# Optimization experiments

Hardware: AMD Instinct MI355X
Metric: run time of the kernel (lower is better)

## Reference

```python
import jax, jax.numpy as jnp
import numpy as np

N_NODES = 100000
N_EDGES = 1600000
N_PAIRS = 200000
IN_C, HID_C, OUT_C = 128, 128, 64


def setup_inputs() -> dict:
    key = jax.random.key(0)
    ks = jax.random.split(key, 10)
    x = jax.random.normal(ks[0], (N_NODES, IN_C), dtype=jnp.float32)
    edge_index = jax.random.randint(ks[1], (2, N_EDGES), 0, N_NODES, dtype=jnp.int64)
    node_i = jax.random.randint(ks[2], (N_PAIRS,), 0, N_NODES, dtype=jnp.int64)
    node_j = jax.random.randint(ks[3], (N_PAIRS,), 0, N_NODES, dtype=jnp.int64)
    def glorot(k, fan_in, fan_out):
        s = jnp.sqrt(6.0 / (fan_in + fan_out))
        return jax.random.uniform(k, (fan_in, fan_out), jnp.float32, -s, s)
    W1 = glorot(ks[4], IN_C, HID_C)
    b1 = jnp.zeros((HID_C,), jnp.float32)
    W2 = glorot(ks[5], HID_C, HID_C)
    b2 = jnp.zeros((HID_C,), jnp.float32)
    W3 = glorot(ks[6], HID_C, OUT_C)
    b3 = jnp.zeros((OUT_C,), jnp.float32)
    return {"x": x, "edge_index": edge_index, "node_i": node_i, "node_j": node_j,
            "W1": W1, "b1": b1, "W2": W2, "b2": b2, "W3": W3, "b3": b3}


def _gcn_layer(h, src, dst, deg_inv, w_e, W, b):
    # h: [N, Cin] -> linear then symmetric-normalized aggregation (with self loops)
    h = h @ W  # [N, Cout]
    msg = h[src] * w_e[:, None]  # [E, Cout] gather + edge weight
    agg = jax.ops.segment_sum(msg, dst, num_segments=N_NODES)
    agg = agg + h * deg_inv[:, None]  # self-loop term: h_i / deg_i
    return agg + b


def reference(x, edge_index, node_i, node_j, W1, b1, W2, b2, W3, b3):
    src, dst = edge_index[0], edge_index[1]
    # GCN normalization with self loops: deg_i = 1 + in-degree
    ones = jnp.ones((N_EDGES,), jnp.float32)
    deg = jax.ops.segment_sum(ones, dst, num_segments=N_NODES) + 1.0
    dinv_sqrt = jax.lax.rsqrt(deg)
    deg_inv = 1.0 / deg
    w_e = dinv_sqrt[src] * dinv_sqrt[dst]  # [E]

    h = _gcn_layer(x, src, dst, deg_inv, w_e, W1, b1)
    h = jax.nn.relu(h)  # dropout is identity in eval mode
    h = _gcn_layer(h, src, dst, deg_inv, w_e, W2, b2)
    h = jax.nn.relu(h)
    h = _gcn_layer(h, src, dst, deg_inv, w_e, W3, b3)

    # dot-product link decode (decode_type=None)
    return jnp.sum(h[node_i] * h[node_j], axis=-1)  # [N_PAIRS]
```

## Files before the change

kernel.cpp:

```cpp
#include <hip/hip_runtime.h>

#define NN 100000
#define NNP 100032
#define NE 1600000
#define NP 200000
#define NBKT 782
#define BCAP 3072
#define BKB 4096

typedef short s16x8 __attribute__((ext_vector_type(8)));
typedef float f32x4 __attribute__((ext_vector_type(4)));

__device__ __forceinline__ unsigned short f2bf(float f) {
  unsigned int u = __float_as_uint(f);
  u += 0x7fffu + ((u >> 16) & 1u);
  return (unsigned short)(u >> 16);
}

__device__ __forceinline__ void upadd(uint u, float& lo, float& hi) {
  lo += __uint_as_float(u << 16);
  hi += __uint_as_float(u & 0xffff0000u);
}

template <int NT>
__device__ __forceinline__ void prepw_dev(const float* __restrict__ W,
                                          uint* __restrict__ Wt, int tid) {
  constexpr int COUT = NT * 16;
  if (tid >= 4 * NT * 64) return;
  int lane = tid & 63, comb = tid >> 6;
  int ks = comb / NT, tl = comb % NT;
  int q = lane >> 4, n = lane & 15;
  uint w[4];
#pragma unroll
  for (int jj = 0; jj < 4; ++jj) {
    int k0 = ks * 32 + q * 8 + 2 * jj;
    uint lo = f2bf(W[k0 * COUT + tl * 16 + n]);
    uint hi = f2bf(W[(k0 + 1) * COUT + tl * 16 + n]);
    w[jj] = lo | (hi << 16);
  }
  ((uint4*)Wt)[comb * 64 + lane] = make_uint4(w[0], w[1], w[2], w[3]);
}

__global__ __launch_bounds__(256) void k_setup(const float* __restrict__ W1,
                                               const float* __restrict__ W2,
                                               const float* __restrict__ W3,
                                               uint* __restrict__ Wt1,
                                               uint* __restrict__ Wt2,
                                               uint* __restrict__ Wt3,
                                               int* __restrict__ gcur) {
  int b = blockIdx.x, t = threadIdx.x;
  if (b < 4) {
    int i = b * 256 + t;
    if (i < 1024) gcur[i] = 0;
  } else if (b < 12) {
    prepw_dev<8>(W1, Wt1, (b - 4) * 256 + t);
  } else if (b < 20) {
    prepw_dev<8>(W2, Wt2, (b - 12) * 256 + t);
  } else {
    prepw_dev<4>(W3, Wt3, (b - 20) * 256 + t);
  }
}

__global__ __launch_bounds__(256) void k_bucket(const int* __restrict__ ei,
                                                int* __restrict__ gcur,
                                                int* __restrict__ aux) {
  __shared__ int cnt[1024];
  __shared__ int scn[1024];
  __shared__ int cur[1024];
  __shared__ int sc[256];
  __shared__ int sorted[BKB];
  __shared__ unsigned short sbkt[BKB];
  const int t = threadIdx.x;
  const int base = blockIdx.x * BKB;

  for (int i = t; i < 1024; i += 256) cnt[i] = 0;
  __syncthreads();

  int pk[16], bk[16];
#pragma unroll
  for (int i = 0; i < 16; ++i) {
    int e = base + t + 256 * i;
    if (e < NE) {
      int src = ei[e], dst = ei[NE + e];
      bk[i] = dst >> 7;
      pk[i] = src | ((dst & 127) << 17);
      atomicAdd(&cnt[bk[i]], 1);
    } else {
      bk[i] = -1;
    }
  }
  __syncthreads();

  int s0 = cnt[4 * t], s1 = cnt[4 * t + 1], s2 = cnt[4 * t + 2], s3 = cnt[4 * t + 3];
  int local = s0 + s1 + s2 + s3;
  sc[t] = local;
  __syncthreads();
  for (int off = 1; off < 256; off <<= 1) {
    int a = (t >= off) ? sc[t - off] : 0;
    __syncthreads();
    sc[t] += a;
    __syncthreads();
  }
  int b0 = sc[t] - local;
  scn[4 * t] = b0;
  scn[4 * t + 1] = b0 + s0;
  scn[4 * t + 2] = b0 + s0 + s1;
  scn[4 * t + 3] = b0 + s0 + s1 + s2;
  cur[4 * t] = scn[4 * t];
  cur[4 * t + 1] = scn[4 * t + 1];
  cur[4 * t + 2] = scn[4 * t + 2];
  cur[4 * t + 3] = scn[4 * t + 3];
  __syncthreads();
  const int tot = sc[255];

#pragma unroll
  for (int i = 0; i < 16; ++i) {
    if (bk[i] >= 0) {
      int pos = atomicAdd(&cur[bk[i]], 1);
      sorted[pos] = pk[i];
      sbkt[pos] = (unsigned short)bk[i];
    }
  }
  __syncthreads();

  for (int b = t; b < 1024; b += 256) {
    int c = cnt[b];
    if (c > 0) cur[b] = b * BCAP + atomicAdd(&gcur[b], c);
  }
  __syncthreads();

  for (int k = t; k < tot; k += 256) {
    int b = sbkt[k];
    aux[cur[b] + (k - scn[b])] = sorted[k];
  }
}

__global__ __launch_bounds__(256) void k_csr(const int* __restrict__ gcur,
                                             const int* __restrict__ aux,
                                             int* __restrict__ row_ptr,
                                             float* __restrict__ dinv,
                                             int* __restrict__ col) {
  __shared__ int red[256];
  __shared__ int c[128];
  __shared__ int cur[128];
  const int b = blockIdx.x, t = threadIdx.x;
  int p = 0;
  for (int i = t; i < b; i += 256) p += gcur[i];
  red[t] = p;
  if (t < 128) c[t] = 0;
  __syncthreads();
  for (int off = 128; off > 0; off >>= 1) {
    if (t < off) red[t] += red[t + off];
    __syncthreads();
  }
  const int base = red[0];
  const int m = gcur[b];
  const int* a = aux + (size_t)b * BCAP;
  __syncthreads();
  for (int k = t; k < m; k += 256) atomicAdd(&c[a[k] >> 17], 1);
  __syncthreads();
  int val = (t < 128) ? c[t] : 0;
  red[t] = val;
  __syncthreads();
  for (int off = 1; off < 128; off <<= 1) {
    int add = (t >= off && t < 128) ? red[t - off] : 0;
    __syncthreads();
    if (t < 128) red[t] += add;
    __syncthreads();
  }
  if (t < 128) {
    int excl = red[t] - val + base;
    int node = b * 128 + t;
    if (node < NN) {
      row_ptr[node] = excl;
      dinv[node] = rsqrtf((float)(val + 1));
      cur[t] = excl;
    }
  }
  if (b == NBKT - 1 && t == 0) row_ptr[NN] = base + m;
  __syncthreads();
  for (int k = t; k < m; k += 256) {
    int pk2 = a[k];
    int pos = atomicAdd(&cur[pk2 >> 17], 1);
    col[pos] = pk2 & 0x1FFFF;
  }
}

__global__ __launch_bounds__(256) void k_gemm1(const float* __restrict__ A,
                                               const uint* __restrict__ Wt,
                                               const float* __restrict__ dinv,
                                               unsigned short* __restrict__ T) {
  constexpr int NT = 8, COUT = 128;
  __shared__ __align__(16) uint Wlds[4 * NT * 64 * 4];
  __shared__ __align__(16) unsigned short Obuf[64 * COUT];
  const int t = threadIdx.x;
  {
    const uint4* src = (const uint4*)Wt;
    uint4* dst = (uint4*)Wlds;
    for (int i = t; i < 4 * NT * 64; i += 256) dst[i] = src[i];
  }
  __syncthreads();

  const int wv = t >> 6, lane = t & 63;
  const int n = lane & 15, quad = lane >> 4;
  const int rbase = blockIdx.x * 64 + wv * 16;

  union AB { uint4 u; s16x8 s; };
  AB a[4];
  {
    int row = rbase + n;
    if (row >= NN) row = NN - 1;
    const float* ap = A + (size_t)row * 128;
#pragma unroll
    for (int ks = 0; ks < 4; ++ks) {
      float4 v0 = *(const float4*)(ap + ks * 32 + quad * 8);
      float4 v1 = *(const float4*)(ap + ks * 32 + quad * 8 + 4);
      a[ks].u.x = (uint)f2bf(v0.x) | ((uint)f2bf(v0.y) << 16);
      a[ks].u.y = (uint)f2bf(v0.z) | ((uint)f2bf(v0.w) << 16);
      a[ks].u.z = (uint)f2bf(v1.x) | ((uint)f2bf(v1.y) << 16);
      a[ks].u.w = (uint)f2bf(v1.z) | ((uint)f2bf(v1.w) << 16);
    }
  }

  f32x4 acc[NT];
#pragma unroll
  for (int tl = 0; tl < NT; ++tl) acc[tl] = (f32x4){0.f, 0.f, 0.f, 0.f};

#pragma unroll
  for (int ks = 0; ks < 4; ++ks) {
#pragma unroll
    for (int tl = 0; tl < NT; ++tl) {
      AB b;
      b.u = *(const uint4*)&Wlds[((ks * NT + tl) * 64 + lane) * 4];
      acc[tl] = __builtin_amdgcn_mfma_f32_16x16x32_bf16(a[ks].s, b.s, acc[tl], 0, 0, 0);
    }
  }

  float4 dv = *(const float4*)(dinv + rbase + quad * 4);
  float dvv[4] = {dv.x, dv.y, dv.z, dv.w};
  unsigned short* ob = Obuf + wv * 16 * COUT;
#pragma unroll
  for (int tl = 0; tl < NT; ++tl)
#pragma unroll
    for (int r = 0; r < 4; ++r)
      ob[(quad * 4 + r) * COUT + tl * 16 + n] = f2bf(acc[tl][r] * dvv[r]);

  uint4* gdst = (uint4*)(T + (size_t)rbase * COUT);
#pragma unroll
  for (int i = 0; i < 4; ++i) {
    int off16 = i * 64 + lane;
    int lrow = (off16 * 8) / COUT;
    uint4 v = make_uint4(0u, 0u, 0u, 0u);
    if (rbase + lrow < NN) v = *(const uint4*)&ob[off16 * 8];
    gdst[off16] = v;
  }
}

template <int COUT>
__global__ __launch_bounds__(256) void k_gg(const int* __restrict__ row_ptr,
                                            const int* __restrict__ col,
                                            const uint4* __restrict__ T4,
                                            const float* __restrict__ dinv,
                                            const float* __restrict__ bias,
                                            const uint4* __restrict__ Wt,
                                            unsigned short* __restrict__ Tout) {
  constexpr int NT = COUT / 16;
  constexpr int TLW = NT / 4;
  constexpr int OSTR = COUT + 8;
  __shared__ __align__(16) uint4 Alds[16 * 17];
  const int t = threadIdx.x, wv = t >> 6, lane = t & 63;
  const int nbase = blockIdx.x * 16;
  const int q = lane >> 4, cl = lane & 15;

#pragma unroll 1
  for (int i = 0; i < 4; ++i) {
    const int node = nbase + wv * 4 + i;
    int s = 0, tend = 0;
    if (node < NN) { s = row_ptr[node]; tend = row_ptr[node + 1]; }
    float acc[8] = {0.f, 0.f, 0.f, 0.f, 0.f, 0.f, 0.f, 0.f};
    if (q == 0) {
      uint4 u = T4[(size_t)node * 16 + cl];
      upadd(u.x, acc[0], acc[1]);
      upadd(u.y, acc[2], acc[3]);
      upadd(u.z, acc[4], acc[5]);
      upadd(u.w, acc[6], acc[7]);
    }
    const int d = tend - s;
    const int nfull = d >> 4;
    int e = s + q;
    for (int it = 0; it < nfull; ++it, e += 16) {
      int c0 = col[e], c1 = col[e + 4], c2 = col[e + 8], c3 = col[e + 12];
      uint4 v0 = T4[(size_t)c0 * 16 + cl];
      uint4 v1 = T4[(size_t)c1 * 16 + cl];
      uint4 v2 = T4[(size_t)c2 * 16 + cl];
      uint4 v3 = T4[(size_t)c3 * 16 + cl];
      upadd(v0.x, acc[0], acc[1]); upadd(v0.y, acc[2], acc[3]);
      upadd(v0.z, acc[4], acc[5]); upadd(v0.w, acc[6], acc[7]);
      upadd(v1.x, acc[0], acc[1]); upadd(v1.y, acc[2], acc[3]);
      upadd(v1.z, acc[4], acc[5]); upadd(v1.w, acc[6], acc[7]);
      upadd(v2.x, acc[0], acc[1]); upadd(v2.y, acc[2], acc[3]);
      upadd(v2.z, acc[4], acc[5]); upadd(v2.w, acc[6], acc[7]);
      upadd(v3.x, acc[0], acc[1]); upadd(v3.y, acc[2], acc[3]);
      upadd(v3.z, acc[4], acc[5]); upadd(v3.w, acc[6], acc[7]);
    }
    if (d & 15) {
      const int m = tend - 1;
      int i0 = e, i1 = e + 4, i2 = e + 8, i3 = e + 12;
      int c0 = col[min(i0, m)], c1 = col[min(i1, m)];
      int c2 = col[min(i2, m)], c3 = col[min(i3, m)];
      c0 = (i0 < tend) ? c0 : NN;
      c1 = (i1 < tend) ? c1 : NN;
      c2 = (i2 < tend) ? c2 : NN;
      c3 = (i3 < tend) ? c3 : NN;
      uint4 v0 = T4[(size_t)c0 * 16 + cl];
      uint4 v1 = T4[(size_t)c1 * 16 + cl];
      uint4 v2 = T4[(size_t)c2 * 16 + cl];
      uint4 v3 = T4[(size_t)c3 * 16 + cl];
      upadd(v0.x, acc[0], acc[1]); upadd(v0.y, acc[2], acc[3]);
      upadd(v0.z, acc[4], acc[5]); upadd(v0.w, acc[6], acc[7]);
      upadd(v1.x, acc[0], acc[1]); upadd(v1.y, acc[2], acc[3]);
      upadd(v1.z, acc[4], acc[5]); upadd(v1.w, acc[6], acc[7]);
      upadd(v2.x, acc[0], acc[1]); upadd(v2.y, acc[2], acc[3]);
      upadd(v2.z, acc[4], acc[5]); upadd(v2.w, acc[6], acc[7]);
      upadd(v3.x, acc[0], acc[1]); upadd(v3.y, acc[2], acc[3]);
      upadd(v3.z, acc[4], acc[5]); upadd(v3.w, acc[6], acc[7]);
    }
#pragma unroll
    for (int k = 0; k < 8; ++k) {
      acc[k] += __shfl_down(acc[k], 16, 64);
      acc[k] += __shfl_down(acc[k], 32, 64);
    }
    if (q == 0) {
      float4 b0 = *(const float4*)&bias[cl * 8];
      float4 b1 = *(const float4*)&bias[cl * 8 + 4];
      float dv = dinv[node];
      float r[8];
      r[0] = fmaxf(fmaf(dv, acc[0], b0.x), 0.f);
      r[1] = fmaxf(fmaf(dv, acc[1], b0.y), 0.f);
      r[2] = fmaxf(fmaf(dv, acc[2], b0.z), 0.f);
      r[3] = fmaxf(fmaf(dv, acc[3], b0.w), 0.f);
      r[4] = fmaxf(fmaf(dv, acc[4], b1.x), 0.f);
      r[5] = fmaxf(fmaf(dv, acc[5], b1.y), 0.f);
      r[6] = fmaxf(fmaf(dv, acc[6], b1.z), 0.f);
      r[7] = fmaxf(fmaf(dv, acc[7], b1.w), 0.f);
      uint4 o;
      o.x = (uint)f2bf(r[0]) | ((uint)f2bf(r[1]) << 16);
      o.y = (uint)f2bf(r[2]) | ((uint)f2bf(r[3]) << 16);
      o.z = (uint)f2bf(r[4]) | ((uint)f2bf(r[5]) << 16);
      o.w = (uint)f2bf(r[6]) | ((uint)f2bf(r[7]) << 16);
      Alds[(wv * 4 + i) * 17 + cl] = o;
    }
  }
  __syncthreads();

  const int n = lane & 15, quad = lane >> 4;
  union AB { uint4 u; s16x8 s; };
  AB a[4];
#pragma unroll
  for (int ks = 0; ks < 4; ++ks) a[ks].u = Alds[n * 17 + ks * 4 + quad];
  f32x4 acc2[TLW];
#pragma unroll
  for (int j = 0; j < TLW; ++j) acc2[j] = (f32x4){0.f, 0.f, 0.f, 0.f};
#pragma unroll
  for (int ks = 0; ks < 4; ++ks) {
#pragma unroll
    for (int j = 0; j < TLW; ++j) {
      int tl = wv * TLW + j;
      AB b;
      b.u = Wt[(ks * NT + tl) * 64 + lane];
      acc2[j] = __builtin_amdgcn_mfma_f32_16x16x32_bf16(a[ks].s, b.s, acc2[j], 0, 0, 0);
    }
  }
  __syncthreads();

  unsigned short* Obuf = (unsigned short*)Alds;
  float4 dv4 = *(const float4*)(dinv + nbase + quad * 4);
  float dvv[4] = {dv4.x, dv4.y, dv4.z, dv4.w};
#pragma unroll
  for (int j = 0; j < TLW; ++j) {
    int tl = wv * TLW + j;
#pragma unroll
    for (int r = 0; r < 4; ++r)
      Obuf[(quad * 4 + r) * OSTR + tl * 16 + n] = f2bf(acc2[j][r] * dvv[r]);
  }
  __syncthreads();

  if constexpr (COUT == 128) {
    int row = t >> 4, c16 = t & 15;
    uint4 v = make_uint4(0u, 0u, 0u, 0u);
    if (nbase + row < NN) v = *(const uint4*)&Obuf[row * OSTR + c16 * 8];
    ((uint4*)(Tout + (size_t)nbase * COUT))[row * 16 + c16] = v;
  } else {
    if (t < 128) {
      int row = t >> 3, c16 = t & 7;
      uint4 v = make_uint4(0u, 0u, 0u, 0u);
      if (nbase + row < NN) v = *(const uint4*)&Obuf[row * OSTR + c16 * 8];
      ((uint4*)(Tout + (size_t)nbase * COUT))[row * 8 + c16] = v;
    }
  }
}

__global__ __launch_bounds__(256) void k_gather3(const int* __restrict__ row_ptr,
                                                 const int* __restrict__ col,
                                                 const uint4* __restrict__ T4,
                                                 uint4* __restrict__ G3) {
  int w = (blockIdx.x * 256 + threadIdx.x) >> 6;
  int lane = threadIdx.x & 63;
  if (w >= NN) return;
  int s = row_ptr[w], tend = row_ptr[w + 1];
  const int g = lane >> 3;
  const int cl = lane & 7;
  float acc[8] = {0.f, 0.f, 0.f, 0.f, 0.f, 0.f, 0.f, 0.f};
  if (g == 0) {
    uint4 u = T4[(size_t)w * 8 + cl];
    upadd(u.x, acc[0], acc[1]);
    upadd(u.y, acc[2], acc[3]);
    upadd(u.z, acc[4], acc[5]);
    upadd(u.w, acc[6], acc[7]);
  }
  const int d = tend - s;
  const int nfull = d >> 4;
  int e = s + g;
  for (int it = 0; it < nfull; ++it, e += 16) {
    int c0 = col[e], c1 = col[e + 8];
    uint4 v0 = T4[(size_t)c0 * 8 + cl];
    uint4 v1 = T4[(size_t)c1 * 8 + cl];
    upadd(v0.x, acc[0], acc[1]); upadd(v0.y, acc[2], acc[3]);
    upadd(v0.z, acc[4], acc[5]); upadd(v0.w, acc[6], acc[7]);
    upadd(v1.x, acc[0], acc[1]); upadd(v1.y, acc[2], acc[3]);
    upadd(v1.z, acc[4], acc[5]); upadd(v1.w, acc[6], acc[7]);
  }
  if (d & 15) {
    const int m = tend - 1;
    int i0 = e, i1 = e + 8;
    int c0 = col[min(i0, m)], c1 = col[min(i1, m)];
    c0 = (i0 < tend) ? c0 : NN;
    c1 = (i1 < tend) ? c1 : NN;
    uint4 v0 = T4[(size_t)c0 * 8 + cl];
    uint4 v1 = T4[(size_t)c1 * 8 + cl];
    upadd(v0.x, acc[0], acc[1]); upadd(v0.y, acc[2], acc[3]);
    upadd(v0.z, acc[4], acc[5]); upadd(v0.w, acc[6], acc[7]);
    upadd(v1.x, acc[0], acc[1]); upadd(v1.y, acc[2], acc[3]);
    upadd(v1.z, acc[4], acc[5]); upadd(v1.w, acc[6], acc[7]);
  }
#pragma unroll
  for (int i = 0; i < 8; ++i) {
    acc[i] += __shfl_down(acc[i], 8, 64);
    acc[i] += __shfl_down(acc[i], 16, 64);
    acc[i] += __shfl_down(acc[i], 32, 64);
  }
  if (g == 0) {
    uint4 o;
    o.x = (uint)f2bf(acc[0]) | ((uint)f2bf(acc[1]) << 16);
    o.y = (uint)f2bf(acc[2]) | ((uint)f2bf(acc[3]) << 16);
    o.z = (uint)f2bf(acc[4]) | ((uint)f2bf(acc[5]) << 16);
    o.w = (uint)f2bf(acc[6]) | ((uint)f2bf(acc[7]) << 16);
    G3[(size_t)w * 8 + cl] = o;
  }
}

__global__ __launch_bounds__(256) void k_decode(const int* __restrict__ ni,
                                                const int* __restrict__ nj,
                                                const uint2* __restrict__ G3,
                                                const float* __restrict__ dinv,
                                                const float* __restrict__ b3,
                                                float* __restrict__ out) {
  int p = blockIdx.x * 16 + (threadIdx.x >> 4);
  int cl = threadIdx.x & 15;
  int i = ni[p], j = nj[p];
  uint2 ui = G3[(size_t)i * 16 + cl];
  uint2 uj = G3[(size_t)j * 16 + cl];
  float4 bb = *(const float4*)&b3[cl * 4];
  float di = dinv[i], dj = dinv[j];
  float gi0 = __uint_as_float(ui.x << 16), gi1 = __uint_as_float(ui.x & 0xffff0000u);
  float gi2 = __uint_as_float(ui.y << 16), gi3 = __uint_as_float(ui.y & 0xffff0000u);
  float gj0 = __uint_as_float(uj.x << 16), gj1 = __uint_as_float(uj.x & 0xffff0000u);
  float gj2 = __uint_as_float(uj.y << 16), gj3 = __uint_as_float(uj.y & 0xffff0000u);
  float v = fmaf(di, gi0, bb.x) * fmaf(dj, gj0, bb.x) +
            fmaf(di, gi1, bb.y) * fmaf(dj, gj1, bb.y) +
            fmaf(di, gi2, bb.z) * fmaf(dj, gj2, bb.z) +
            fmaf(di, gi3, bb.w) * fmaf(dj, gj3, bb.w);
  v += __shfl_xor(v, 1, 64);
  v += __shfl_xor(v, 2, 64);
  v += __shfl_xor(v, 4, 64);
  v += __shfl_xor(v, 8, 64);
  if (cl == 0) out[p] = v;
}

extern "C" void kernel_launch(void* const* d_in, const int* in_sizes, int n_in,
                              void* d_out, int out_size, void* d_ws, size_t ws_size,
                              hipStream_t stream) {
  const float* x  = (const float*)d_in[0];
  const int*   ei = (const int*)d_in[1];
  const int*   ni = (const int*)d_in[2];
  const int*   nj = (const int*)d_in[3];
  const float* W1 = (const float*)d_in[4];
  const float* b1 = (const float*)d_in[5];
  const float* W2 = (const float*)d_in[6];
  const float* b2 = (const float*)d_in[7];
  const float* W3 = (const float*)d_in[8];
  const float* b3 = (const float*)d_in[9];
  float* out = (float*)d_out;

  float* dinv    = (float*)d_ws;
  int*   row_ptr = (int*)(dinv + 102400);
  int*   gcur    = row_ptr + 102400;
  int*   col     = gcur + 1024;
  uint*  Wt1     = (uint*)(col + NE);
  uint*  Wt2     = Wt1 + 8192;
  uint*  Wt3     = Wt2 + 8192;
  uint*  Tbf     = Wt3 + 4096;
  uint*  T2      = Tbf + (size_t)NNP * 64;
  uint*  G3      = T2 + (size_t)NNP * 64;
  int*   aux     = (int*)G3;

  k_setup<<<24, 256, 0, stream>>>(W1, W2, W3, Wt1, Wt2, Wt3, gcur);
  k_bucket<<<(NE + BKB - 1) / BKB, 256, 0, stream>>>(ei, gcur, aux);
  k_csr<<<NBKT, 256, 0, stream>>>(gcur, aux, row_ptr, dinv, col);

  const int GB = NNP / 64;
  const int FB = NNP / 16;
  const int GATB = (NN * 64 + 255) / 256;

  k_gemm1<<<GB, 256, 0, stream>>>(x, Wt1, dinv, (unsigned short*)Tbf);
  k_gg<128><<<FB, 256, 0, stream>>>(row_ptr, col, (const uint4*)Tbf, dinv, b1,
                                    (const uint4*)Wt2, (unsigned short*)T2);
  k_gg<64><<<FB, 256, 0, stream>>>(row_ptr, col, (const uint4*)T2, dinv, b2,
                                   (const uint4*)Wt3, (unsigned short*)Tbf);
  k_gather3<<<GATB, 256, 0, stream>>>(row_ptr, col, (const uint4*)Tbf, (uint4*)G3);
  k_decode<<<NP / 16, 256, 0, stream>>>(ni, nj, (const uint2*)G3, dinv, b3, out);
}
```

Measured before the change: 330.5 us.

## Assign one lane subgroup per node in gather kernels with packed-add accumulation

The neighbour-aggregation loops in k_gg and k_gather3 are rewritten. Each node is now handled by a 16-lane group (or an 8-lane group in k_gather3) that walks its whole edge list, instead of a full wave splitting the edges and then combining partial sums with cross-lane shuffles. A shared gath helper unrolls by 8 with the next batch of col indices loaded ahead, uses 32-bit shifted address arithmetic, and accumulates with inline v_pk_add_f32. The aim is to remove shuffle reductions and idle tail lanes and to put more loads in flight. The trade-offs are divergence when node degrees within a wave differ, col reads that are no longer coalesced and run past the end of the row, and reliance on the padded row NN being zero.

```diff
diff --git a/kernel.cpp b/kernel.cpp
--- a/kernel.cpp
+++ b/kernel.cpp
@@ -10,6 +10,7 @@
 
 typedef short s16x8 __attribute__((ext_vector_type(8)));
 typedef float f32x4 __attribute__((ext_vector_type(4)));
+typedef float f32x2 __attribute__((ext_vector_type(2)));
 
 __device__ __forceinline__ unsigned short f2bf(float f) {
   unsigned int u = __float_as_uint(f);
@@ -17,9 +18,73 @@
   return (unsigned short)(u >> 16);
 }
 
-__device__ __forceinline__ void upadd(uint u, float& lo, float& hi) {
-  lo += __uint_as_float(u << 16);
-  hi += __uint_as_float(u & 0xffff0000u);
+__device__ __forceinline__ void pkadd(f32x2& a, uint u) {
+  f32x2 v;
+  v.x = __uint_as_float(u << 16);
+  v.y = __uint_as_float(u & 0xffff0000u);
+  asm("v_pk_add_f32 %0, %0, %1" : "+v"(a) : "v"(v));
+}
+
+__device__ __forceinline__ void rowadd(uint4 v, f32x2* a) {
+  pkadd(a[0], v.x);
+  pkadd(a[1], v.y);
+  pkadd(a[2], v.z);
+  pkadd(a[3], v.w);
+}
+
+template <int RSH>
+__device__ __forceinline__ void gath(const int* __restrict__ col,
+                                     const char* __restrict__ Tb, int s,
+                                     int tend, uint co, f32x2* acc) {
+  const int d = tend - s;
+  const int nfull = d >> 3;
+  const int rem = d & 7;
+  int e = s;
+  int c[8];
+#pragma unroll
+  for (int j = 0; j < 8; ++j) c[j] = col[e + j];
+#pragma unroll 1
+  for (int it = 0; it < nfull; ++it) {
+    uint4 v0 = *(const uint4*)(Tb + (((uint)c[0] << RSH) | co));
+    uint4 v1 = *(const uint4*)(Tb + (((uint)c[1] << RSH) | co));
+    uint4 v2 = *(const uint4*)(Tb + (((uint)c[2] << RSH) | co));
+    uint4 v3 = *(const uint4*)(Tb + (((uint)c[3] << RSH) | co));
+    uint4 v4 = *(const uint4*)(Tb + (((uint)c[4] << RSH) | co));
+    uint4 v5 = *(const uint4*)(Tb + (((uint)c[5] << RSH) | co));
+    uint4 v6 = *(const uint4*)(Tb + (((uint)c[6] << RSH) | co));
+    uint4 v7 = *(const uint4*)(Tb + (((uint)c[7] << RSH) | co));
+    e += 8;
+#pragma unroll
+    for (int j = 0; j < 8; ++j) c[j] = col[e + j];
+    rowadd(v0, acc);
+    rowadd(v1, acc);
+    rowadd(v2, acc);
+    rowadd(v3, acc);
+    rowadd(v4, acc);
+    rowadd(v5, acc);
+    rowadd(v6, acc);
+    rowadd(v7, acc);
+  }
+  if (rem) {
+#pragma unroll
+    for (int j = 0; j < 8; ++j) c[j] = (j < rem) ? c[j] : NN;
+    uint4 v0 = *(const uint4*)(Tb + (((uint)c[0] << RSH) | co));
+    uint4 v1 = *(const uint4*)(Tb + (((uint)c[1] << RSH) | co));
+    uint4 v2 = *(const uint4*)(Tb + (((uint)c[2] << RSH) | co));
+    uint4 v3 = *(const uint4*)(Tb + (((uint)c[3] << RSH) | co));
+    uint4 v4 = *(const uint4*)(Tb + (((uint)c[4] << RSH) | co));
+    uint4 v5 = *(const uint4*)(Tb + (((uint)c[5] << RSH) | co));
+    uint4 v6 = *(const uint4*)(Tb + (((uint)c[6] << RSH) | co));
+    uint4 v7 = *(const uint4*)(Tb + (((uint)c[7] << RSH) | co));
+    rowadd(v0, acc);
+    rowadd(v1, acc);
+    rowadd(v2, acc);
+    rowadd(v3, acc);
+    rowadd(v4, acc);
+    rowadd(v5, acc);
+    rowadd(v6, acc);
+    rowadd(v7, acc);
+  }
 }
 
 template <int NT>
@@ -272,84 +337,40 @@
   const int nbase = blockIdx.x * 16;
   const int q = lane >> 4, cl = lane & 15;
 
-#pragma unroll 1
-  for (int i = 0; i < 4; ++i) {
-    const int node = nbase + wv * 4 + i;
-    int s = 0, tend = 0;
-    if (node < NN) { s = row_ptr[node]; tend = row_ptr[node + 1]; }
-    float acc[8] = {0.f, 0.f, 0.f, 0.f, 0.f, 0.f, 0.f, 0.f};
-    if (q == 0) {
-      uint4 u = T4[(size_t)node * 16 + cl];
-      upadd(u.x, acc[0], acc[1]);
-      upadd(u.y, acc[2], acc[3]);
-      upadd(u.z, acc[4], acc[5]);
-      upadd(u.w, acc[6], acc[7]);
-    }
-    const int d = tend - s;
-    const int nfull = d >> 4;
-    int e = s + q;
-    for (int it = 0; it < nfull; ++it, e += 16) {
-      int c0 = col[e], c1 = col[e + 4], c2 = col[e + 8], c3 = col[e + 12];
-      uint4 v0 = T4[(size_t)c0 * 16 + cl];
-      uint4 v1 = T4[(size_t)c1 * 16 + cl];
-      uint4 v2 = T4[(size_t)c2 * 16 + cl];
-      uint4 v3 = T4[(size_t)c3 * 16 + cl];
-      upadd(v0.x, acc[0], acc[1]); upadd(v0.y, acc[2], acc[3]);
-      upadd(v0.z, acc[4], acc[5]); upadd(v0.w, acc[6], acc[7]);
-      upadd(v1.x, acc[0], acc[1]); upadd(v1.y, acc[2], acc[3]);
-      upadd(v1.z, acc[4], acc[5]); upadd(v1.w, acc[6], acc[7]);
-      upadd(v2.x, acc[0], acc[1]); upadd(v2.y, acc[2], acc[3]);
-      upadd(v2.z, acc[4], acc[5]); upadd(v2.w, acc[6], acc[7]);
-      upadd(v3.x, acc[0], acc[1]); upadd(v3.y, acc[2], acc[3]);
-      upadd(v3.z, acc[4], acc[5]); upadd(v3.w, acc[6], acc[7]);
-    }
-    if (d & 15) {
-      const int m = tend - 1;
-      int i0 = e, i1 = e + 4, i2 = e + 8, i3 = e + 12;
-      int c0 = col[min(i0, m)], c1 = col[min(i1, m)];
-      int c2 = col[min(i2, m)], c3 = col[min(i3, m)];
-      c0 = (i0 < tend) ? c0 : NN;
-      c1 = (i1 < tend) ? c1 : NN;
-      c2 = (i2 < tend) ? c2 : NN;
-      c3 = (i3 < tend) ? c3 : NN;
-      uint4 v0 = T4[(size_t)c0 * 16 + cl];
-      uint4 v1 = T4[(size_t)c1 * 16 + cl];
-      uint4 v2 = T4[(size_t)c2 * 16 + cl];
-      uint4 v3 = T4[(size_t)c3 * 16 + cl];
-      upadd(v0.x, acc[0], acc[1]); upadd(v0.y, acc[2], acc[3]);
-      upadd(v0.z, acc[4], acc[5]); upadd(v0.w, acc[6], acc[7]);
-      upadd(v1.x, acc[0], acc[1]); upadd(v1.y, acc[2], acc[3]);
-      upadd(v1.z, acc[4], acc[5]); upadd(v1.w, acc[6], acc[7]);
-      upadd(v2.x, acc[0], acc[1]); upadd(v2.y, acc[2], acc[3]);
-      upadd(v2.z, acc[4], acc[5]); upadd(v2.w, acc[6], acc[7]);
-      upadd(v3.x, acc[0], acc[1]); upadd(v3.y, acc[2], acc[3]);
-      upadd(v3.z, acc[4], acc[5]); upadd(v3.w, acc[6], acc[7]);
-    }
-#pragma unroll
-    for (int k = 0; k < 8; ++k) {
-      acc[k] += __shfl_down(acc[k], 16, 64);
-      acc[k] += __shfl_down(acc[k], 32, 64);
-    }
-    if (q == 0) {
-      float4 b0 = *(const float4*)&bias[cl * 8];
-      float4 b1 = *(const float4*)&bias[cl * 8 + 4];
-      float dv = dinv[node];
-      float r[8];
-      r[0] = fmaxf(fmaf(dv, acc[0], b0.x), 0.f);
-      r[1] = fmaxf(fmaf(dv, acc[1], b0.y), 0.f);
-      r[2] = fmaxf(fmaf(dv, acc[2], b0.z), 0.f);
-      r[3] = fmaxf(fmaf(dv, acc[3], b0.w), 0.f);
-      r[4] = fmaxf(fmaf(dv, acc[4], b1.x), 0.f);
-      r[5] = fmaxf(fmaf(dv, acc[5], b1.y), 0.f);
-      r[6] = fmaxf(fmaf(dv, acc[6], b1.z), 0.f);
-      r[7] = fmaxf(fmaf(dv, acc[7], b1.w), 0.f);
-      uint4 o;
-      o.x = (uint)f2bf(r[0]) | ((uint)f2bf(r[1]) << 16);
-      o.y = (uint)f2bf(r[2]) | ((uint)f2bf(r[3]) << 16);
-      o.z = (uint)f2bf(r[4]) | ((uint)f2bf(r[5]) << 16);
-      o.w = (uint)f2bf(r[6]) | ((uint)f2bf(r[7]) << 16);
-      Alds[(wv * 4 + i) * 17 + cl] = o;
-    }
+  const int node = nbase + wv * 4 + q;
+  int s = 0, tend = 0;
+  if (node < NN) {
+    s = row_ptr[node];
+    tend = row_ptr[node + 1];
+  }
+  const char* Tb = (const char*)T4;
+  const uint co = (uint)cl << 4;
+  f32x2 acc[4];
+  acc[0] = (f32x2){0.f, 0.f};
+  acc[1] = (f32x2){0.f, 0.f};
+  acc[2] = (f32x2){0.f, 0.f};
+  acc[3] = (f32x2){0.f, 0.f};
+  rowadd(*(const uint4*)(Tb + (((uint)node << 8) | co)), acc);
+  gath<8>(col, Tb, s, tend, co, acc);
+
+  {
+    float dv = dinv[node];
+    float4 b0 = *(const float4*)&bias[cl * 8];
+    float4 b1 = *(const float4*)&bias[cl * 8 + 4];
+    float r0 = fmaxf(fmaf(dv, acc[0].x, b0.x), 0.f);
+    float r1 = fmaxf(fmaf(dv, acc[0].y, b0.y), 0.f);
+    float r2 = fmaxf(fmaf(dv, acc[1].x, b0.z), 0.f);
+    float r3 = fmaxf(fmaf(dv, acc[1].y, b0.w), 0.f);
+    float r4 = fmaxf(fmaf(dv, acc[2].x, b1.x), 0.f);
+    float r5 = fmaxf(fmaf(dv, acc[2].y, b1.y), 0.f);
+    float r6 = fmaxf(fmaf(dv, acc[3].x, b1.z), 0.f);
+    float r7 = fmaxf(fmaf(dv, acc[3].y, b1.w), 0.f);
+    uint4 o;
+    o.x = (uint)f2bf(r0) | ((uint)f2bf(r1) << 16);
+    o.y = (uint)f2bf(r2) | ((uint)f2bf(r3) << 16);
+    o.z = (uint)f2bf(r4) | ((uint)f2bf(r5) << 16);
+    o.w = (uint)f2bf(r6) | ((uint)f2bf(r7) << 16);
+    Alds[(wv * 4 + q) * 17 + cl] = o;
   }
   __syncthreads();
 
@@ -404,59 +425,27 @@
                                                  const int* __restrict__ col,
                                                  const uint4* __restrict__ T4,
                                                  uint4* __restrict__ G3) {
-  int w = (blockIdx.x * 256 + threadIdx.x) >> 6;
-  int lane = threadIdx.x & 63;
-  if (w >= NN) return;
-  int s = row_ptr[w], tend = row_ptr[w + 1];
-  const int g = lane >> 3;
-  const int cl = lane & 7;
-  float acc[8] = {0.f, 0.f, 0.f, 0.f, 0.f, 0.f, 0.f, 0.f};
-  if (g == 0) {
-    uint4 u = T4[(size_t)w * 8 + cl];
-    upadd(u.x, acc[0], acc[1]);
-    upadd(u.y, acc[2], acc[3]);
-    upadd(u.z, acc[4], acc[5]);
-    upadd(u.w, acc[6], acc[7]);
-  }
-  const int d = tend - s;
-  const int nfull = d >> 4;
-  int e = s + g;
-  for (int it = 0; it < nfull; ++it, e += 16) {
-    int c0 = col[e], c1 = col[e + 8];
-    uint4 v0 = T4[(size_t)c0 * 8 + cl];
-    uint4 v1 = T4[(size_t)c1 * 8 + cl];
-    upadd(v0.x, acc[0], acc[1]); upadd(v0.y, acc[2], acc[3]);
-    upadd(v0.z, acc[4], acc[5]); upadd(v0.w, acc[6], acc[7]);
-    upadd(v1.x, acc[0], acc[1]); upadd(v1.y, acc[2], acc[3]);
-    upadd(v1.z, acc[4], acc[5]); upadd(v1.w, acc[6], acc[7]);
-  }
-  if (d & 15) {
-    const int m = tend - 1;
-    int i0 = e, i1 = e + 8;
-    int c0 = col[min(i0, m)], c1 = col[min(i1, m)];
-    c0 = (i0 < tend) ? c0 : NN;
-    c1 = (i1 < tend) ? c1 : NN;
-    uint4 v0 = T4[(size_t)c0 * 8 + cl];
-    uint4 v1 = T4[(size_t)c1 * 8 + cl];
-    upadd(v0.x, acc[0], acc[1]); upadd(v0.y, acc[2], acc[3]);
-    upadd(v0.z, acc[4], acc[5]); upadd(v0.w, acc[6], acc[7]);
-    upadd(v1.x, acc[0], acc[1]); upadd(v1.y, acc[2], acc[3]);
-    upadd(v1.z, acc[4], acc[5]); upadd(v1.w, acc[6], acc[7]);
-  }
-#pragma unroll
-  for (int i = 0; i < 8; ++i) {
-    acc[i] += __shfl_down(acc[i], 8, 64);
-    acc[i] += __shfl_down(acc[i], 16, 64);
-    acc[i] += __shfl_down(acc[i], 32, 64);
-  }
-  if (g == 0) {
-    uint4 o;
-    o.x = (uint)f2bf(acc[0]) | ((uint)f2bf(acc[1]) << 16);
-    o.y = (uint)f2bf(acc[2]) | ((uint)f2bf(acc[3]) << 16);
-    o.z = (uint)f2bf(acc[4]) | ((uint)f2bf(acc[5]) << 16);
-    o.w = (uint)f2bf(acc[6]) | ((uint)f2bf(acc[7]) << 16);
-    G3[(size_t)w * 8 + cl] = o;
-  }
+  const int wid = (blockIdx.x * 256 + threadIdx.x) >> 6;
+  const int lane = threadIdx.x & 63;
+  const int g = lane >> 3, cl = lane & 7;
+  const int node = wid * 8 + g;
+  if (node >= NN) return;
+  int s = row_ptr[node], tend = row_ptr[node + 1];
+  const char* Tb = (const char*)T4;
+  const uint co = (uint)cl << 4;
+  f32x2 acc[4];
+  acc[0] = (f32x2){0.f, 0.f};
+  acc[1] = (f32x2){0.f, 0.f};
+  acc[2] = (f32x2){0.f, 0.f};
+  acc[3] = (f32x2){0.f, 0.f};
+  rowadd(*(const uint4*)(Tb + (((uint)node << 7) | co)), acc);
+  gath<7>(col, Tb, s, tend, co, acc);
+  uint4 o;
+  o.x = (uint)f2bf(acc[0].x) | ((uint)f2bf(acc[0].y) << 16);
+  o.y = (uint)f2bf(acc[1].x) | ((uint)f2bf(acc[1].y) << 16);
+  o.z = (uint)f2bf(acc[2].x) | ((uint)f2bf(acc[2].y) << 16);
+  o.w = (uint)f2bf(acc[3].x) | ((uint)f2bf(acc[3].y) << 16);
+  G3[(size_t)node * 8 + cl] = o;
 }
 
 __global__ __launch_bounds__(256) void k_decode(const int* __restrict__ ni,
@@ -520,7 +509,7 @@
 
   const int GB = NNP / 64;
   const int FB = NNP / 16;
-  const int GATB = (NN * 64 + 255) / 256;
+  const int GATB = NN / 32;
 
   k_gemm1<<<GB, 256, 0, stream>>>(x, Wt1, dinv, (unsigned short*)Tbf);
   k_gg<128><<<FB, 256, 0, stream>>>(row_ptr, col, (const uint4*)Tbf, dinv, b1,
```

After: 305.5 us. 1.08x faster.
